# Performance work log

Hardware: AMD Instinct MI355X
Metric: run time of the kernel (lower is better)

## Reference

```python
import jax, jax.numpy as jnp
import numpy as np

KH, KW = 3, 3
STRIDE, PAD, DIL = 1, 1, 1
HEADS, GROUPS, CLIP = 12, 12, 2
C, H, W = 288, 64, 64
B = 2


def _bilinear(img, ys, xs):
    # img: (c, H, W); ys, xs: (K, H, W) fractional sample coords -> (c, K, H, W)
    # DCN-style bilinear with zero outside the image (per-corner validity).
    Hh, Ww = img.shape[1], img.shape[2]
    y0 = jnp.floor(ys)
    x0 = jnp.floor(xs)
    dy = ys - y0
    dx = xs - x0
    out = jnp.zeros((img.shape[0],) + ys.shape, dtype=img.dtype)
    for oy, wy in ((y0, 1.0 - dy), (y0 + 1.0, dy)):
        for ox, wx in ((x0, 1.0 - dx), (x0 + 1.0, dx)):
            valid = (oy >= 0) & (oy <= Hh - 1) & (ox >= 0) & (ox <= Ww - 1)
            yi = jnp.clip(oy, 0, Hh - 1).astype(jnp.int32)
            xi = jnp.clip(ox, 0, Ww - 1).astype(jnp.int32)
            out = out + img[:, yi, xi] * (wy * wx * valid.astype(img.dtype))[None]
    return out


_sample = jax.vmap(jax.vmap(jax.vmap(_bilinear)))  # over (B, T, G)


def _linear5d(x, Wm, b):
    # x: (n, d, c, h, w); Wm: (out, in); torch nn.Linear applied channel-last
    return jnp.einsum('ndchw,oc->ndohw', x, Wm) + b[None, None, :, None, None]


def _deform_attn(q, kv, offset):
    # q: (B,1,C,H,W); kv: (B,T,2C,H,W); offset: (B, T*G*K*2, H, W)
    K = KH * KW
    hd = C // HEADS
    cpg = C // GROUPS
    scale = hd ** -0.5
    A = H * W
    off = offset.reshape(B, CLIP, GROUPS, K, 2, H, W)
    ky = jnp.repeat(jnp.arange(KH), KW).astype(q.dtype)   # (K,)
    kx = jnp.tile(jnp.arange(KW), KH).astype(q.dtype)
    py = jnp.arange(H, dtype=q.dtype)
    px = jnp.arange(W, dtype=q.dtype)
    base_y = ky[:, None, None] * DIL - PAD + py[None, :, None] * STRIDE  # (K,H,1)
    base_x = kx[:, None, None] * DIL - PAD + px[None, None, :] * STRIDE  # (K,1,W)
    ys = base_y + off[..., 0, :, :]  # (B,T,G,K,H,W)
    xs = base_x + off[..., 1, :, :]
    # split kv into k/v, group channels so k and v share per-group offsets
    k_in = kv[:, :, :C].reshape(B, CLIP, GROUPS, cpg, H, W)
    v_in = kv[:, :, C:].reshape(B, CLIP, GROUPS, cpg, H, W)
    kv_g = jnp.concatenate([k_in, v_in], axis=3)          # (B,T,G,2*cpg,H,W)
    samp = _sample(kv_g, ys, xs)                          # (B,T,G,2*cpg,K,H,W)
    k_s = samp[:, :, :, :cpg]
    v_s = samp[:, :, :, cpg:]
    # (B,T,G,cpg,K,H,W) -> (B,HEADS,hd,T*K,A)
    def to_heads(t):
        t = t.reshape(B, CLIP, C, K, A).transpose(0, 2, 1, 3, 4)
        return t.reshape(B, HEADS, hd, CLIP * K, A)
    k_s = to_heads(k_s)
    v_s = to_heads(v_s)
    q_r = q.reshape(B, HEADS, hd, A) * jnp.asarray(scale, q.dtype)
    attn = jnp.einsum('bhda,bhdka->bhka', q_r, k_s)       # (B,HEADS,T*K,A)
    attn = jax.nn.softmax(attn, axis=2)
    out = jnp.einsum('bhka,bhdka->bhda', attn, v_s)
    return out.reshape(B, 1, C, H, W)


def setup_inputs() -> dict:
    key = jax.random.key(0)
    ks = jax.random.split(key, 16)
    s = 0.02
    inp = {
        'q': jax.random.normal(ks[0], (B, 1, C, H, W), jnp.float32),
        'k': jax.random.normal(ks[1], (B, CLIP, C, H, W), jnp.float32),
        'v': jax.random.normal(ks[2], (B, CLIP, C, H, W), jnp.float32),
        'offset': jax.random.normal(ks[3], (B, CLIP * GROUPS * KH * KW * 2, H, W), jnp.float32),
        'Wq': jax.random.normal(ks[4], (C, C), jnp.float32) * s,
        'bq': jnp.zeros((C,), jnp.float32),
        'Wk': jax.random.normal(ks[5], (C, C), jnp.float32) * s,
        'bk': jnp.zeros((C,), jnp.float32),
        'Wv': jax.random.normal(ks[6], (C, C), jnp.float32) * s,
        'bv': jnp.zeros((C,), jnp.float32),
        'W1': jax.random.normal(ks[7], (2 * C, C), jnp.float32) * s,
        'b1': jnp.zeros((2 * C,), jnp.float32),
        'W2': jax.random.normal(ks[8], (C, 2 * C), jnp.float32) * s,
        'b2': jnp.zeros((C,), jnp.float32),
    }
    return inp


def reference(q, k, v, offset, Wq, bq, Wk, bk, Wv, bv, W1, b1, W2, b2):
    qp = _linear5d(q, Wq, bq)
    kv = jnp.concatenate([_linear5d(k, Wk, bk), _linear5d(v, Wv, bv)], axis=2)
    o = _deform_attn(qp, kv, offset)
    # MLP (channel-last), residual: v = v + mlp(v)
    x = jnp.moveaxis(o, 2, -1)
    x = jnp.einsum('ndhwc,oc->ndhwo', x, W1) + b1
    x = jax.nn.gelu(x, approximate=False)
    x = jnp.einsum('ndhwc,oc->ndhwo', x, W2) + b2
    return o + jnp.moveaxis(x, -1, 2)
```

## Files before the change

kernel.cpp:

```cpp
#include <hip/hip_runtime.h>

#define AREA 4096

typedef short short8 __attribute__((ext_vector_type(8)));
typedef float f32x4 __attribute__((ext_vector_type(4)));

__device__ __forceinline__ unsigned bf16_rn(float x) {
    unsigned u = __builtin_bit_cast(unsigned, x);
    u += 0x7fffu + ((u >> 16) & 1u);
    return u >> 16;
}
__device__ __forceinline__ float bflo(unsigned u) { return __builtin_bit_cast(float, u << 16); }
__device__ __forceinline__ float bfhi(unsigned u) { return __builtin_bit_cast(float, u & 0xffff0000u); }
__device__ __forceinline__ float gelu_f(float x) {
    return 0.5f * x * (1.f + erff(x * 0.70710678118654752f));
}

#define OFF_Q 0
#define OFF_K (162 * 64)
#define OFF_V (324 * 64)
#define OFF_1 (486 * 64)
#define OFF_2 (810 * 64)

__global__ __launch_bounds__(256) void prep_kernel(
    const float* __restrict__ q, const float* __restrict__ k,
    const float* __restrict__ v,
    const float* __restrict__ Wq, const float* __restrict__ Wk,
    const float* __restrict__ Wv, const float* __restrict__ W1,
    const float* __restrict__ W2,
    unsigned* __restrict__ xq, unsigned* __restrict__ xk,
    unsigned* __restrict__ xv, uint4* __restrict__ wp)
{
    if (blockIdx.y < 3) {
        const float* src; unsigned* dst; int nimg;
        switch (blockIdx.y) {
            case 0: src = q; dst = xq; nimg = 2; break;
            case 1: src = k; dst = xk; nimg = 4; break;
            default:src = v; dst = xv; nimg = 4; break;
        }
        int idx = blockIdx.x * 256 + threadIdx.x;
        if (idx >= nimg * AREA * 36) return;
        int a = idx & (AREA - 1);
        int rest = idx >> 12;
        int oct = rest % 36;
        int n = rest / 36;
        const float* s = src + ((long)n * 288 + oct * 8) * AREA + a;
        uint4 u;
        u.x = bf16_rn(s[0])        | (bf16_rn(s[AREA])     << 16);
        u.y = bf16_rn(s[2 * AREA]) | (bf16_rn(s[3 * AREA]) << 16);
        u.z = bf16_rn(s[4 * AREA]) | (bf16_rn(s[5 * AREA]) << 16);
        u.w = bf16_rn(s[6 * AREA]) | (bf16_rn(s[7 * AREA]) << 16);
        *(uint4*)(dst + ((long)n * AREA + a) * 144 + oct * 4) = u;
    } else {
        int gw = blockIdx.x * 4 + (threadIdx.x >> 6);
        if (gw >= 1134) return;
        int lane = threadIdx.x & 63;
        const float* W; int Cin, KS, local, off;
        if      (gw < 162) { W = Wq; Cin = 288; KS = 9;  local = gw;       off = OFF_Q; }
        else if (gw < 324) { W = Wk; Cin = 288; KS = 9;  local = gw - 162; off = OFF_K; }
        else if (gw < 486) { W = Wv; Cin = 288; KS = 9;  local = gw - 324; off = OFF_V; }
        else if (gw < 810) { W = W1; Cin = 288; KS = 9;  local = gw - 486; off = OFF_1; }
        else               { W = W2; Cin = 576; KS = 18; local = gw - 810; off = OFF_2; }
        int ot = local / KS, ks = local - ot * KS;
        int o = ot * 16 + (lane & 15);
        int c0 = ks * 32 + ((lane >> 4) << 3);
        const float4* wr = (const float4*)(W + (long)o * Cin + c0);
        float4 f0 = wr[0], f1 = wr[1];
        uint4 u;
        u.x = bf16_rn(f0.x) | (bf16_rn(f0.y) << 16);
        u.y = bf16_rn(f0.z) | (bf16_rn(f0.w) << 16);
        u.z = bf16_rn(f1.x) | (bf16_rn(f1.y) << 16);
        u.w = bf16_rn(f1.z) | (bf16_rn(f1.w) << 16);
        wp[(long)off + (long)local * 64 + lane] = u;
    }
}

__global__ __launch_bounds__(256) void proj_qkv(
    const unsigned* __restrict__ xq, const unsigned* __restrict__ xk,
    const unsigned* __restrict__ xv, const uint4* __restrict__ wp,
    const float* __restrict__ bq, const float* __restrict__ bk,
    const float* __restrict__ bv, unsigned* __restrict__ qp_u,
    unsigned* __restrict__ kv_u)
{
    const int z = blockIdx.z;
    const unsigned* Xt; const uint4* Wp; const float* bias;
    int outmode, voff, n;
    if (z < 2)      { Xt = xq; Wp = wp + OFF_Q; bias = bq; outmode = 1; voff = 0;  n = z; }
    else if (z < 6) { Xt = xk; Wp = wp + OFF_K; bias = bk; outmode = 2; voff = 0;  n = z - 2; }
    else            { Xt = xv; Wp = wp + OFF_V; bias = bv; outmode = 2; voff = 12; n = z - 6; }

    const int tid = threadIdx.x;
    const int lane = tid & 63;
    const int w = tid >> 6;
    const int ot0 = blockIdx.y * 2;
    const int pw = blockIdx.x * 256 + w * 64;
    const int lcol = lane & 15;
    const int lrow = lane >> 4;

    const uint4* xrow[4];
#pragma unroll
    for (int s = 0; s < 4; ++s)
        xrow[s] = (const uint4*)(Xt + ((long)n * AREA + pw + s * 16 + lcol) * 144);
    const uint4* wa0 = Wp + (long)ot0 * 9 * 64 + lane;
    const uint4* wa1 = Wp + (long)(ot0 + 1) * 9 * 64 + lane;

    f32x4 acc[2][4];
#pragma unroll
    for (int m = 0; m < 2; ++m)
#pragma unroll
        for (int s = 0; s < 4; ++s) acc[m][s] = (f32x4){0.f, 0.f, 0.f, 0.f};

    for (int ks = 0; ks < 9; ++ks) {
        uint4 a0 = wa0[(long)ks * 64];
        uint4 a1 = wa1[(long)ks * 64];
        uint4 b[4];
#pragma unroll
        for (int s = 0; s < 4; ++s) b[s] = xrow[s][ks * 4 + lrow];
        short8 A0 = __builtin_bit_cast(short8, a0);
        short8 A1 = __builtin_bit_cast(short8, a1);
#pragma unroll
        for (int s = 0; s < 4; ++s) {
            short8 B = __builtin_bit_cast(short8, b[s]);
            acc[0][s] = __builtin_amdgcn_mfma_f32_16x16x32_bf16(A0, B, acc[0][s], 0, 0, 0);
            acc[1][s] = __builtin_amdgcn_mfma_f32_16x16x32_bf16(A1, B, acc[1][s], 0, 0, 0);
        }
    }

#pragma unroll
    for (int m = 0; m < 2; ++m) {
        const int obase = (ot0 + m) * 16 + lrow * 4;
        const float b0 = bias[obase], b1 = bias[obase + 1];
        const float b2 = bias[obase + 2], b3 = bias[obase + 3];
#pragma unroll
        for (int s = 0; s < 4; ++s) {
            const int pcol = pw + s * 16 + lcol;
            f32x4 a = acc[m][s];
            float v0 = a[0] + b0, v1 = a[1] + b1, v2 = a[2] + b2, v3 = a[3] + b3;
            uint2 st;
            st.x = bf16_rn(v0) | (bf16_rn(v1) << 16);
            st.y = bf16_rn(v2) | (bf16_rn(v3) << 16);
            if (outmode == 1) {
                *(uint2*)(qp_u + ((long)n * AREA + pcol) * 144 + (obase >> 1)) = st;
            } else {
                int g = obase / 24, d0 = obase % 24;
                unsigned* ub = kv_u +
                    ((long)(n * 12 + g) * AREA + pcol) * 24 + voff + (d0 >> 1);
                *(uint2*)ub = st;
            }
        }
    }
}

template<int OUT>
__global__ __launch_bounds__(256) void proj_mfma(
    const unsigned* __restrict__ Xt, const uint4* __restrict__ Wp,
    const float* __restrict__ bias, void* __restrict__ outp,
    const float* __restrict__ res, int KS, int RSu)
{
    const int tid = threadIdx.x;
    const int lane = tid & 63;
    const int w = tid >> 6;
    const int n = blockIdx.z;
    const int ot0 = blockIdx.y * 2;
    const int pw = blockIdx.x * 256 + w * 64;
    const int lcol = lane & 15;
    const int lrow = lane >> 4;

    const uint4* xrow[4];
#pragma unroll
    for (int s = 0; s < 4; ++s)
        xrow[s] = (const uint4*)(Xt + ((long)n * AREA + pw + s * 16 + lcol) * RSu);
    const uint4* wa0 = Wp + (long)ot0 * KS * 64 + lane;
    const uint4* wa1 = Wp + (long)(ot0 + 1) * KS * 64 + lane;

    f32x4 acc[2][4];
#pragma unroll
    for (int m = 0; m < 2; ++m)
#pragma unroll
        for (int s = 0; s < 4; ++s) acc[m][s] = (f32x4){0.f, 0.f, 0.f, 0.f};

    for (int ks = 0; ks < KS; ++ks) {
        uint4 a0 = wa0[(long)ks * 64];
        uint4 a1 = wa1[(long)ks * 64];
        uint4 b[4];
#pragma unroll
        for (int s = 0; s < 4; ++s) b[s] = xrow[s][ks * 4 + lrow];
        short8 A0 = __builtin_bit_cast(short8, a0);
        short8 A1 = __builtin_bit_cast(short8, a1);
#pragma unroll
        for (int s = 0; s < 4; ++s) {
            short8 B = __builtin_bit_cast(short8, b[s]);
            acc[0][s] = __builtin_amdgcn_mfma_f32_16x16x32_bf16(A0, B, acc[0][s], 0, 0, 0);
            acc[1][s] = __builtin_amdgcn_mfma_f32_16x16x32_bf16(A1, B, acc[1][s], 0, 0, 0);
        }
    }

#pragma unroll
    for (int m = 0; m < 2; ++m) {
        const int obase = (ot0 + m) * 16 + lrow * 4;
        const float b0 = bias[obase], b1 = bias[obase + 1];
        const float b2 = bias[obase + 2], b3 = bias[obase + 3];
#pragma unroll
        for (int s = 0; s < 4; ++s) {
            const int pcol = pw + s * 16 + lcol;
            f32x4 a = acc[m][s];
            float v0 = a[0] + b0, v1 = a[1] + b1, v2 = a[2] + b2, v3 = a[3] + b3;
            if (OUT == 3) {
                v0 = gelu_f(v0); v1 = gelu_f(v1); v2 = gelu_f(v2); v3 = gelu_f(v3);
                uint2 st;
                st.x = bf16_rn(v0) | (bf16_rn(v1) << 16);
                st.y = bf16_rn(v2) | (bf16_rn(v3) << 16);
                *(uint2*)((unsigned*)outp + ((long)n * AREA + pcol) * 288 + (obase >> 1)) = st;
            } else {
                float* fb = (float*)outp;
                float vals[4] = {v0, v1, v2, v3};
#pragma unroll
                for (int r = 0; r < 4; ++r) {
                    long addr = ((long)n * 288 + obase + r) * AREA + pcol;
                    fb[addr] = vals[r] + res[addr];
                }
            }
        }
    }
}

__global__ __launch_bounds__(256) void deform_attn_kernel(
    const unsigned* __restrict__ qp, const unsigned* __restrict__ kv,
    const float* __restrict__ offs, float* __restrict__ o,
    unsigned* __restrict__ ot)
{
    const int bid = blockIdx.x;
    const int swz = (bid & 7) * 192 + (bid >> 3);
    const int t = swz * 256 + threadIdx.x;
    const int role = t & 1;
    const int clip = (t >> 1) & 1;
    const int site = t >> 2;
    const int a = site & (AREA - 1);
    const int g = (site >> 12) % 12;
    const int b = site / (12 * AREA);
    const int py = a >> 6, px = a & 63;
    const float scale = 0.20412414523193150818f;

    float qv[24];
    {
        const uint4* qb = (const uint4*)(qp + ((long)b * AREA + a) * 144 + g * 12);
        uint4 q0 = qb[0], q1 = qb[1], q2 = qb[2];
        unsigned uq[12] = {q0.x, q0.y, q0.z, q0.w, q1.x, q1.y, q1.z, q1.w,
                           q2.x, q2.y, q2.z, q2.w};
#pragma unroll
        for (int j = 0; j < 12; ++j) {
            qv[2 * j]     = bflo(uq[j]) * scale;
            qv[2 * j + 1] = bfhi(uq[j]) * scale;
        }
    }

    float m = -1e30f, l = 0.f;
    float outv[24];
#pragma unroll
    for (int d = 0; d < 24; ++d) outv[d] = 0.f;

    const unsigned* __restrict__ cb =
        kv + (long)((b * 2 + clip) * 12 + g) * AREA * 24 + role * 12;
    const float* __restrict__ obase =
        offs + ((long)b * 432 + (clip * 12 + g) * 18) * AREA;
#pragma unroll 1
    for (int k = 0; k < 9; ++k) {
        float oy = obase[(long)(2 * k) * AREA + a];
        float ox = obase[(long)(2 * k + 1) * AREA + a];
        int ky = k / 3, kx = k - ky * 3;
        float ys = (float)(py + ky - 1) + oy;
        float xs_ = (float)(px + kx - 1) + ox;
        float y0f = floorf(ys), x0f = floorf(xs_);
        float dy = ys - y0f, dx = xs_ - x0f;
        float wy[2] = {1.f - dy, dy};
        float wx[2] = {1.f - dx, dx};
        long  idx4[4];
        float w4[4];
#pragma unroll
        for (int cy = 0; cy < 2; ++cy) {
            float yc = y0f + (float)cy;
            bool vy = (yc >= 0.f) && (yc <= 63.f);
            int yi = (int)fminf(fmaxf(yc, 0.f), 63.f);
#pragma unroll
            for (int cx = 0; cx < 2; ++cx) {
                float xc = x0f + (float)cx;
                bool vx = (xc >= 0.f) && (xc <= 63.f);
                int xi = (int)fminf(fmaxf(xc, 0.f), 63.f);
                w4[cy * 2 + cx] = wy[cy] * wx[cx] * ((vy && vx) ? 1.f : 0.f);
                idx4[cy * 2 + cx] = (long)(yi * 64 + xi) * 24;
            }
        }
        float xs[24];
#pragma unroll
        for (int j = 0; j < 24; ++j) xs[j] = 0.f;
        float sh = 0.f;
#pragma unroll
        for (int c = 0; c < 4; ++c) {
            const uint4* pc = (const uint4*)(cb + idx4[c]);
            uint4 u0 = pc[0], u1 = pc[1], u2 = pc[2];
            unsigned uu[12] = {u0.x, u0.y, u0.z, u0.w,
                               u1.x, u1.y, u1.z, u1.w,
                               u2.x, u2.y, u2.z, u2.w};
            float w = w4[c];
            float d = 0.f;
#pragma unroll
            for (int j = 0; j < 12; ++j) {
                float lo = bflo(uu[j]), hi = bfhi(uu[j]);
                d = fmaf(qv[2 * j], lo, d);
                d = fmaf(qv[2 * j + 1], hi, d);
                xs[2 * j]     = fmaf(w, lo, xs[2 * j]);
                xs[2 * j + 1] = fmaf(w, hi, xs[2 * j + 1]);
            }
            sh = fmaf(w, d, sh);
        }
        float sx = __shfl_xor(sh, 1);
        float s = role ? sx : sh;
        float mn = fmaxf(m, s);
        float corr = __expf(m - mn);
        float p = __expf(s - mn);
        l = l * corr + p;
        m = mn;
#pragma unroll
        for (int j = 0; j < 24; ++j)
            outv[j] = fmaf(outv[j], corr, p * xs[j]);
    }

    float mo  = __shfl_xor(m, 2);
    float lo2 = __shfl_xor(l, 2);
    float mn = fmaxf(m, mo);
    float fs = __expf(m - mn), fo = __expf(mo - mn);
    float lm = l * fs + lo2 * fo;
    float inv = 1.f / lm;
#pragma unroll
    for (int d = 0; d < 24; ++d) {
        float ovo = __shfl_xor(outv[d], 2);
        outv[d] = (outv[d] * fs + ovo * fo) * inv;
    }

    if (role == 1 && clip == 0) {
        float ov[24];
#pragma unroll
        for (int d = 0; d < 24; ++d) {
            ov[d] = outv[d];
            o[((long)b * 288 + g * 24 + d) * AREA + a] = ov[d];
        }
        unsigned* tb = ot + ((long)b * AREA + a) * 144 + g * 12;
        uint4 s0, s1, s2;
        s0.x = bf16_rn(ov[0])  | (bf16_rn(ov[1])  << 16);
        s0.y = bf16_rn(ov[2])  | (bf16_rn(ov[3])  << 16);
        s0.z = bf16_rn(ov[4])  | (bf16_rn(ov[5])  << 16);
        s0.w = bf16_rn(ov[6])  | (bf16_rn(ov[7])  << 16);
        s1.x = bf16_rn(ov[8])  | (bf16_rn(ov[9])  << 16);
        s1.y = bf16_rn(ov[10]) | (bf16_rn(ov[11]) << 16);
        s1.z = bf16_rn(ov[12]) | (bf16_rn(ov[13]) << 16);
        s1.w = bf16_rn(ov[14]) | (bf16_rn(ov[15]) << 16);
        s2.x = bf16_rn(ov[16]) | (bf16_rn(ov[17]) << 16);
        s2.y = bf16_rn(ov[18]) | (bf16_rn(ov[19]) << 16);
        s2.z = bf16_rn(ov[20]) | (bf16_rn(ov[21]) << 16);
        s2.w = bf16_rn(ov[22]) | (bf16_rn(ov[23]) << 16);
        ((uint4*)tb)[0] = s0; ((uint4*)tb)[1] = s1; ((uint4*)tb)[2] = s2;
    }
}

extern "C" void kernel_launch(void* const* d_in, const int* in_sizes, int n_in,
                              void* d_out, int out_size, void* d_ws, size_t ws_size,
                              hipStream_t stream) {
    const float* q      = (const float*)d_in[0];
    const float* k      = (const float*)d_in[1];
    const float* v      = (const float*)d_in[2];
    const float* offset = (const float*)d_in[3];
    const float* Wq     = (const float*)d_in[4];
    const float* bq     = (const float*)d_in[5];
    const float* Wk     = (const float*)d_in[6];
    const float* bk     = (const float*)d_in[7];
    const float* Wv     = (const float*)d_in[8];
    const float* bv     = (const float*)d_in[9];
    const float* W1     = (const float*)d_in[10];
    const float* b1     = (const float*)d_in[11];
    const float* W2     = (const float*)d_in[12];
    const float* b2     = (const float*)d_in[13];
    float* out = (float*)d_out;
    float* ws  = (float*)d_ws;

    unsigned* qp_u = (unsigned*)ws;
    unsigned* kv_u = (unsigned*)(ws + 2359296);
    unsigned* xq   = (unsigned*)(ws + 7077888);
    unsigned* xk   = (unsigned*)(ws + 8257536);
    unsigned* xv   = (unsigned*)(ws + 10616832);
    uint4*    wp   = (uint4*)(ws + 12976128);
    unsigned* x1   = xk;
    unsigned* o_t  = xv;

    prep_kernel<<<dim3(2304, 4), dim3(256), 0, stream>>>(
        q, k, v, Wq, Wk, Wv, W1, W2, xq, xk, xv, wp);
    proj_qkv<<<dim3(16, 9, 10), dim3(256), 0, stream>>>(
        xq, xk, xv, wp, bq, bk, bv, qp_u, kv_u);
    deform_attn_kernel<<<dim3(1536), dim3(256), 0, stream>>>(
        qp_u, kv_u, offset, out, o_t);
    proj_mfma<3><<<dim3(16, 18, 2), dim3(256), 0, stream>>>(
        o_t, wp + OFF_1, b1, x1, nullptr, 9, 144);
    proj_mfma<0><<<dim3(16, 9, 2), dim3(256), 0, stream>>>(
        x1, wp + OFF_2, b2, out, out, 18, 288);
}
```

Baseline: 134.0 us.

## Fuse bf16 conversion of inputs and weights into projection GEMMs via LDS staging

Removes the separate prep kernel. The projection kernels now read the fp32 weights and the fp32 q/k/v activations directly, convert them to bf16 and stage them in LDS, transposing activations on the fly. This drops one launch and the write and re-read of the intermediate bf16 buffers, at the cost of redundant weight conversion in every block and extra syncs per k-step in the QKV GEMM. The deform-attention sampling loop is also partially unrolled.

```diff
diff --git a/kernel.cpp b/kernel.cpp
--- a/kernel.cpp
+++ b/kernel.cpp
@@ -16,93 +16,63 @@
     return 0.5f * x * (1.f + erff(x * 0.70710678118654752f));
 }
 
-#define OFF_Q 0
-#define OFF_K (162 * 64)
-#define OFF_V (324 * 64)
-#define OFF_1 (486 * 64)
-#define OFF_2 (810 * 64)
-
-__global__ __launch_bounds__(256) void prep_kernel(
+template<int CIN>
+__device__ __forceinline__ void stage_A(const float* __restrict__ Wrow0,
+                                        unsigned* lds_a, int tid) {
+    const int AW = CIN / 2 + 4;
+    for (int i = tid; i < 32 * CIN / 4; i += 256) {
+        int o = i / (CIN / 4);
+        int c4 = i - o * (CIN / 4);
+        float4 f = *(const float4*)(Wrow0 + (long)o * CIN + c4 * 4);
+        lds_a[o * AW + c4 * 2]     = bf16_rn(f.x) | (bf16_rn(f.y) << 16);
+        lds_a[o * AW + c4 * 2 + 1] = bf16_rn(f.z) | (bf16_rn(f.w) << 16);
+    }
+}
+
+__device__ __forceinline__ void stage_B(const float* __restrict__ Xbase,
+                                        unsigned* lds_b, int tid) {
+#pragma unroll
+    for (int j = 0; j < 4; ++j) {
+        int cpair = j * 4 + (tid >> 6);
+        int px0 = (tid & 63) * 4;
+        const float* r0 = Xbase + (long)(2 * cpair) * AREA + px0;
+        float4 a = *(const float4*)r0;
+        float4 b = *(const float4*)(r0 + AREA);
+        lds_b[(px0 + 0) * 20 + cpair] = bf16_rn(a.x) | (bf16_rn(b.x) << 16);
+        lds_b[(px0 + 1) * 20 + cpair] = bf16_rn(a.y) | (bf16_rn(b.y) << 16);
+        lds_b[(px0 + 2) * 20 + cpair] = bf16_rn(a.z) | (bf16_rn(b.z) << 16);
+        lds_b[(px0 + 3) * 20 + cpair] = bf16_rn(a.w) | (bf16_rn(b.w) << 16);
+    }
+}
+
+__global__ __launch_bounds__(256) void proj_qkv2(
     const float* __restrict__ q, const float* __restrict__ k,
     const float* __restrict__ v,
     const float* __restrict__ Wq, const float* __restrict__ Wk,
-    const float* __restrict__ Wv, const float* __restrict__ W1,
-    const float* __restrict__ W2,
-    unsigned* __restrict__ xq, unsigned* __restrict__ xk,
-    unsigned* __restrict__ xv, uint4* __restrict__ wp)
+    const float* __restrict__ Wv,
+    const float* __restrict__ bq, const float* __restrict__ bk,
+    const float* __restrict__ bv,
+    unsigned* __restrict__ qp_u, unsigned* __restrict__ kv_u)
 {
-    if (blockIdx.y < 3) {
-        const float* src; unsigned* dst; int nimg;
-        switch (blockIdx.y) {
-            case 0: src = q; dst = xq; nimg = 2; break;
-            case 1: src = k; dst = xk; nimg = 4; break;
-            default:src = v; dst = xv; nimg = 4; break;
-        }
-        int idx = blockIdx.x * 256 + threadIdx.x;
-        if (idx >= nimg * AREA * 36) return;
-        int a = idx & (AREA - 1);
-        int rest = idx >> 12;
-        int oct = rest % 36;
-        int n = rest / 36;
-        const float* s = src + ((long)n * 288 + oct * 8) * AREA + a;
-        uint4 u;
-        u.x = bf16_rn(s[0])        | (bf16_rn(s[AREA])     << 16);
-        u.y = bf16_rn(s[2 * AREA]) | (bf16_rn(s[3 * AREA]) << 16);
-        u.z = bf16_rn(s[4 * AREA]) | (bf16_rn(s[5 * AREA]) << 16);
-        u.w = bf16_rn(s[6 * AREA]) | (bf16_rn(s[7 * AREA]) << 16);
-        *(uint4*)(dst + ((long)n * AREA + a) * 144 + oct * 4) = u;
-    } else {
-        int gw = blockIdx.x * 4 + (threadIdx.x >> 6);
-        if (gw >= 1134) return;
-        int lane = threadIdx.x & 63;
-        const float* W; int Cin, KS, local, off;
-        if      (gw < 162) { W = Wq; Cin = 288; KS = 9;  local = gw;       off = OFF_Q; }
-        else if (gw < 324) { W = Wk; Cin = 288; KS = 9;  local = gw - 162; off = OFF_K; }
-        else if (gw < 486) { W = Wv; Cin = 288; KS = 9;  local = gw - 324; off = OFF_V; }
-        else if (gw < 810) { W = W1; Cin = 288; KS = 9;  local = gw - 486; off = OFF_1; }
-        else               { W = W2; Cin = 576; KS = 18; local = gw - 810; off = OFF_2; }
-        int ot = local / KS, ks = local - ot * KS;
-        int o = ot * 16 + (lane & 15);
-        int c0 = ks * 32 + ((lane >> 4) << 3);
-        const float4* wr = (const float4*)(W + (long)o * Cin + c0);
-        float4 f0 = wr[0], f1 = wr[1];
-        uint4 u;
-        u.x = bf16_rn(f0.x) | (bf16_rn(f0.y) << 16);
-        u.y = bf16_rn(f0.z) | (bf16_rn(f0.w) << 16);
-        u.z = bf16_rn(f1.x) | (bf16_rn(f1.y) << 16);
-        u.w = bf16_rn(f1.z) | (bf16_rn(f1.w) << 16);
-        wp[(long)off + (long)local * 64 + lane] = u;
-    }
-}
-
-__global__ __launch_bounds__(256) void proj_qkv(
-    const unsigned* __restrict__ xq, const unsigned* __restrict__ xk,
-    const unsigned* __restrict__ xv, const uint4* __restrict__ wp,
-    const float* __restrict__ bq, const float* __restrict__ bk,
-    const float* __restrict__ bv, unsigned* __restrict__ qp_u,
-    unsigned* __restrict__ kv_u)
-{
+    __shared__ unsigned lds_a[32 * 148];
+    __shared__ unsigned lds_b[256 * 20];
     const int z = blockIdx.z;
-    const unsigned* Xt; const uint4* Wp; const float* bias;
+    const float* Xf; const float* W; const float* bias;
     int outmode, voff, n;
-    if (z < 2)      { Xt = xq; Wp = wp + OFF_Q; bias = bq; outmode = 1; voff = 0;  n = z; }
-    else if (z < 6) { Xt = xk; Wp = wp + OFF_K; bias = bk; outmode = 2; voff = 0;  n = z - 2; }
-    else            { Xt = xv; Wp = wp + OFF_V; bias = bv; outmode = 2; voff = 12; n = z - 6; }
+    if (z < 2)      { Xf = q; W = Wq; bias = bq; outmode = 1; voff = 0;  n = z; }
+    else if (z < 6) { Xf = k; W = Wk; bias = bk; outmode = 2; voff = 0;  n = z - 2; }
+    else            { Xf = v; W = Wv; bias = bv; outmode = 2; voff = 12; n = z - 6; }
 
     const int tid = threadIdx.x;
     const int lane = tid & 63;
     const int w = tid >> 6;
     const int ot0 = blockIdx.y * 2;
-    const int pw = blockIdx.x * 256 + w * 64;
+    const int pwb = blockIdx.x * 256;
     const int lcol = lane & 15;
     const int lrow = lane >> 4;
-
-    const uint4* xrow[4];
-#pragma unroll
-    for (int s = 0; s < 4; ++s)
-        xrow[s] = (const uint4*)(Xt + ((long)n * AREA + pw + s * 16 + lcol) * 144);
-    const uint4* wa0 = Wp + (long)ot0 * 9 * 64 + lane;
-    const uint4* wa1 = Wp + (long)(ot0 + 1) * 9 * 64 + lane;
+    const int AW = 148;
+
+    stage_A<288>(W + (long)blockIdx.y * 32 * 288, lds_a, tid);
 
     f32x4 acc[2][4];
 #pragma unroll
@@ -110,17 +80,19 @@
 #pragma unroll
         for (int s = 0; s < 4; ++s) acc[m][s] = (f32x4){0.f, 0.f, 0.f, 0.f};
 
+    const float* Xn = Xf + (long)n * 288 * AREA + pwb;
     for (int ks = 0; ks < 9; ++ks) {
-        uint4 a0 = wa0[(long)ks * 64];
-        uint4 a1 = wa1[(long)ks * 64];
-        uint4 b[4];
-#pragma unroll
-        for (int s = 0; s < 4; ++s) b[s] = xrow[s][ks * 4 + lrow];
+        __syncthreads();
+        stage_B(Xn + (long)(ks * 32) * AREA, lds_b, tid);
+        __syncthreads();
+        uint4 a0 = *(const uint4*)&lds_a[(0 * 16 + lcol) * AW + ks * 16 + lrow * 4];
+        uint4 a1 = *(const uint4*)&lds_a[(1 * 16 + lcol) * AW + ks * 16 + lrow * 4];
         short8 A0 = __builtin_bit_cast(short8, a0);
         short8 A1 = __builtin_bit_cast(short8, a1);
 #pragma unroll
         for (int s = 0; s < 4; ++s) {
-            short8 B = __builtin_bit_cast(short8, b[s]);
+            uint4 bb = *(const uint4*)&lds_b[(w * 64 + s * 16 + lcol) * 20 + lrow * 4];
+            short8 B = __builtin_bit_cast(short8, bb);
             acc[0][s] = __builtin_amdgcn_mfma_f32_16x16x32_bf16(A0, B, acc[0][s], 0, 0, 0);
             acc[1][s] = __builtin_amdgcn_mfma_f32_16x16x32_bf16(A1, B, acc[1][s], 0, 0, 0);
         }
@@ -133,7 +105,7 @@
         const float b2 = bias[obase + 2], b3 = bias[obase + 3];
 #pragma unroll
         for (int s = 0; s < 4; ++s) {
-            const int pcol = pw + s * 16 + lcol;
+            const int pcol = pwb + w * 64 + s * 16 + lcol;
             f32x4 a = acc[m][s];
             float v0 = a[0] + b0, v1 = a[1] + b1, v2 = a[2] + b2, v3 = a[3] + b3;
             uint2 st;
@@ -143,20 +115,20 @@
                 *(uint2*)(qp_u + ((long)n * AREA + pcol) * 144 + (obase >> 1)) = st;
             } else {
                 int g = obase / 24, d0 = obase % 24;
-                unsigned* ub = kv_u +
-                    ((long)(n * 12 + g) * AREA + pcol) * 24 + voff + (d0 >> 1);
-                *(uint2*)ub = st;
+                *(uint2*)(kv_u + ((long)(n * 12 + g) * AREA + pcol) * 24 + voff + (d0 >> 1)) = st;
             }
         }
     }
 }
 
-template<int OUT>
-__global__ __launch_bounds__(256) void proj_mfma(
-    const unsigned* __restrict__ Xt, const uint4* __restrict__ Wp,
+template<int OUT, int CIN>
+__global__ __launch_bounds__(256) void proj_ffn(
+    const unsigned* __restrict__ Xu, const float* __restrict__ W,
     const float* __restrict__ bias, void* __restrict__ outp,
-    const float* __restrict__ res, int KS, int RSu)
+    const float* __restrict__ res, int RSu)
 {
+    const int AW = CIN / 2 + 4;
+    __shared__ unsigned lds_a[32 * (CIN / 2 + 4)];
     const int tid = threadIdx.x;
     const int lane = tid & 63;
     const int w = tid >> 6;
@@ -166,12 +138,13 @@
     const int lcol = lane & 15;
     const int lrow = lane >> 4;
 
+    stage_A<CIN>(W + (long)blockIdx.y * 32 * CIN, lds_a, tid);
+    __syncthreads();
+
     const uint4* xrow[4];
 #pragma unroll
     for (int s = 0; s < 4; ++s)
-        xrow[s] = (const uint4*)(Xt + ((long)n * AREA + pw + s * 16 + lcol) * RSu);
-    const uint4* wa0 = Wp + (long)ot0 * KS * 64 + lane;
-    const uint4* wa1 = Wp + (long)(ot0 + 1) * KS * 64 + lane;
+        xrow[s] = (const uint4*)(Xu + ((long)n * AREA + pw + s * 16 + lcol) * RSu);
 
     f32x4 acc[2][4];
 #pragma unroll
@@ -179,17 +152,14 @@
 #pragma unroll
         for (int s = 0; s < 4; ++s) acc[m][s] = (f32x4){0.f, 0.f, 0.f, 0.f};
 
-    for (int ks = 0; ks < KS; ++ks) {
-        uint4 a0 = wa0[(long)ks * 64];
-        uint4 a1 = wa1[(long)ks * 64];
-        uint4 b[4];
-#pragma unroll
-        for (int s = 0; s < 4; ++s) b[s] = xrow[s][ks * 4 + lrow];
+    for (int ks = 0; ks < CIN / 32; ++ks) {
+        uint4 a0 = *(const uint4*)&lds_a[(0 * 16 + lcol) * AW + ks * 16 + lrow * 4];
+        uint4 a1 = *(const uint4*)&lds_a[(1 * 16 + lcol) * AW + ks * 16 + lrow * 4];
         short8 A0 = __builtin_bit_cast(short8, a0);
         short8 A1 = __builtin_bit_cast(short8, a1);
 #pragma unroll
         for (int s = 0; s < 4; ++s) {
-            short8 B = __builtin_bit_cast(short8, b[s]);
+            short8 B = __builtin_bit_cast(short8, xrow[s][ks * 4 + lrow]);
             acc[0][s] = __builtin_amdgcn_mfma_f32_16x16x32_bf16(A0, B, acc[0][s], 0, 0, 0);
             acc[1][s] = __builtin_amdgcn_mfma_f32_16x16x32_bf16(A1, B, acc[1][s], 0, 0, 0);
         }
@@ -263,7 +233,7 @@
         kv + (long)((b * 2 + clip) * 12 + g) * AREA * 24 + role * 12;
     const float* __restrict__ obase =
         offs + ((long)b * 432 + (clip * 12 + g) * 18) * AREA;
-#pragma unroll 1
+#pragma unroll 3
     for (int k = 0; k < 9; ++k) {
         float oy = obase[(long)(2 * k) * AREA + a];
         float ox = obase[(long)(2 * k + 1) * AREA + a];
@@ -384,21 +354,15 @@
 
     unsigned* qp_u = (unsigned*)ws;
     unsigned* kv_u = (unsigned*)(ws + 2359296);
-    unsigned* xq   = (unsigned*)(ws + 7077888);
-    unsigned* xk   = (unsigned*)(ws + 8257536);
-    unsigned* xv   = (unsigned*)(ws + 10616832);
-    uint4*    wp   = (uint4*)(ws + 12976128);
-    unsigned* x1   = xk;
-    unsigned* o_t  = xv;
-
-    prep_kernel<<<dim3(2304, 4), dim3(256), 0, stream>>>(
-        q, k, v, Wq, Wk, Wv, W1, W2, xq, xk, xv, wp);
-    proj_qkv<<<dim3(16, 9, 10), dim3(256), 0, stream>>>(
-        xq, xk, xv, wp, bq, bk, bv, qp_u, kv_u);
+    unsigned* o_t  = (unsigned*)(ws + 8257536);
+    unsigned* x1   = (unsigned*)(ws + 10616832);
+
+    proj_qkv2<<<dim3(16, 9, 10), dim3(256), 0, stream>>>(
+        q, k, v, Wq, Wk, Wv, bq, bk, bv, qp_u, kv_u);
     deform_attn_kernel<<<dim3(1536), dim3(256), 0, stream>>>(
         qp_u, kv_u, offset, out, o_t);
-    proj_mfma<3><<<dim3(16, 18, 2), dim3(256), 0, stream>>>(
-        o_t, wp + OFF_1, b1, x1, nullptr, 9, 144);
-    proj_mfma<0><<<dim3(16, 9, 2), dim3(256), 0, stream>>>(
-        x1, wp + OFF_2, b2, out, out, 18, 288);
-}
+    proj_ffn<3, 288><<<dim3(16, 18, 2), dim3(256), 0, stream>>>(
+        o_t, W1, b1, x1, nullptr, 144);
+    proj_ffn<0, 576><<<dim3(16, 9, 2), dim3(256), 0, stream>>>(
+        x1, W2, b2, out, out, 288);
+}
```

Result: slower. 165.4 us (+23.4%).

## Split deformable attention into LDS-staged logits pass and separate value-sum pass

Applied to the files above, without the earlier changes.

The fused deformable-attention kernel is split in two. The first kernel stages one half of a group's key slab (12 channels times 4096 pixels) in shared memory and computes bilinear-sampled partial logits from LDS into a global buffer. The second kernel sums the halves, runs a non-online softmax over the 9 taps per clip, and gathers values from a separate V buffer. K and V are written as separate layouts by the projection kernel. This replaces scattered global gathers for K with LDS gathers and removes the online-softmax rescaling. In exchange it adds a logits round-trip through global memory, repeats the offset and bilinear work in both kernels, adds one more launch, and uses 1024-thread blocks with a large LDS footprint.

```diff
diff --git a/kernel.cpp b/kernel.cpp
--- a/kernel.cpp
+++ b/kernel.cpp
@@ -14,6 +14,30 @@
 __device__ __forceinline__ float bfhi(unsigned u) { return __builtin_bit_cast(float, u & 0xffff0000u); }
 __device__ __forceinline__ float gelu_f(float x) {
     return 0.5f * x * (1.f + erff(x * 0.70710678118654752f));
+}
+
+__device__ __forceinline__ void bilin(int k, int py, int px, float oy, float ox,
+                                      int* idx4, float* w4) {
+    int ky = k / 3, kx = k - ky * 3;
+    float ys = (float)(py + ky - 1) + oy;
+    float xs = (float)(px + kx - 1) + ox;
+    float y0f = floorf(ys), x0f = floorf(xs);
+    float dy = ys - y0f, dx = xs - x0f;
+    float wy[2] = {1.f - dy, dy}, wx[2] = {1.f - dx, dx};
+#pragma unroll
+    for (int cy = 0; cy < 2; ++cy) {
+        float yc = y0f + (float)cy;
+        bool vy = (yc >= 0.f) && (yc <= 63.f);
+        int yi = (int)fminf(fmaxf(yc, 0.f), 63.f);
+#pragma unroll
+        for (int cx = 0; cx < 2; ++cx) {
+            float xc = x0f + (float)cx;
+            bool vx = (xc >= 0.f) && (xc <= 63.f);
+            int xi = (int)fminf(fmaxf(xc, 0.f), 63.f);
+            w4[cy * 2 + cx] = wy[cy] * wx[cx] * ((vy && vx) ? 1.f : 0.f);
+            idx4[cy * 2 + cx] = yi * 64 + xi;
+        }
+    }
 }
 
 #define OFF_Q 0
@@ -80,14 +104,14 @@
     const unsigned* __restrict__ xv, const uint4* __restrict__ wp,
     const float* __restrict__ bq, const float* __restrict__ bk,
     const float* __restrict__ bv, unsigned* __restrict__ qp_u,
-    unsigned* __restrict__ kv_u)
+    unsigned* __restrict__ k_u, unsigned* __restrict__ v_u)
 {
     const int z = blockIdx.z;
     const unsigned* Xt; const uint4* Wp; const float* bias;
-    int outmode, voff, n;
-    if (z < 2)      { Xt = xq; Wp = wp + OFF_Q; bias = bq; outmode = 1; voff = 0;  n = z; }
-    else if (z < 6) { Xt = xk; Wp = wp + OFF_K; bias = bk; outmode = 2; voff = 0;  n = z - 2; }
-    else            { Xt = xv; Wp = wp + OFF_V; bias = bv; outmode = 2; voff = 12; n = z - 6; }
+    int outmode, n;
+    if (z < 2)      { Xt = xq; Wp = wp + OFF_Q; bias = bq; outmode = 0; n = z; }
+    else if (z < 6) { Xt = xk; Wp = wp + OFF_K; bias = bk; outmode = 1; n = z - 2; }
+    else            { Xt = xv; Wp = wp + OFF_V; bias = bv; outmode = 2; n = z - 6; }
 
     const int tid = threadIdx.x;
     const int lane = tid & 63;
@@ -139,13 +163,17 @@
             uint2 st;
             st.x = bf16_rn(v0) | (bf16_rn(v1) << 16);
             st.y = bf16_rn(v2) | (bf16_rn(v3) << 16);
-            if (outmode == 1) {
+            if (outmode == 0) {
                 *(uint2*)(qp_u + ((long)n * AREA + pcol) * 144 + (obase >> 1)) = st;
+            } else if (outmode == 1) {
+                int g = obase / 24, d0 = obase % 24;
+                int half = d0 >= 12 ? 1 : 0;
+                int slab = n * 12 + g;
+                *(uint2*)(k_u + ((long)(slab * 2 + half) * AREA + pcol) * 6
+                          + ((d0 % 12) >> 1)) = st;
             } else {
                 int g = obase / 24, d0 = obase % 24;
-                unsigned* ub = kv_u +
-                    ((long)(n * 12 + g) * AREA + pcol) * 24 + voff + (d0 >> 1);
-                *(uint2*)ub = st;
+                *(uint2*)(v_u + ((long)(n * 12 + g) * AREA + pcol) * 12 + (d0 >> 1)) = st;
             }
         }
     }
@@ -224,140 +252,157 @@
     }
 }
 
-__global__ __launch_bounds__(256) void deform_attn_kernel(
-    const unsigned* __restrict__ qp, const unsigned* __restrict__ kv,
+__global__ __launch_bounds__(1024) void attn_logits(
+    const unsigned* __restrict__ qp, const unsigned* __restrict__ k_u,
+    const float* __restrict__ offs, float* __restrict__ lg)
+{
+    __shared__ unsigned kl[AREA * 6];
+    const int bid = blockIdx.x;
+    const int lid = (bid & 7) * 48 + (bid >> 3);
+    const int chunk = lid & 3;
+    const int half = (lid >> 2) & 1;
+    const int slab = lid >> 3;
+    const int g = slab % 12;
+    const int bc = slab / 12;
+    const int b = bc >> 1, clip = bc & 1;
+    const int tid = threadIdx.x;
+
+    const unsigned* ks = k_u + (long)(slab * 2 + half) * AREA * 6;
+#pragma unroll
+    for (int i = 0; i < 4; ++i) {
+        int px = i * 1024 + tid;
+        uint2 a0 = *(const uint2*)(ks + (long)px * 6);
+        uint2 a1 = *(const uint2*)(ks + (long)px * 6 + 2);
+        uint2 a2 = *(const uint2*)(ks + (long)px * 6 + 4);
+        *(uint2*)&kl[px * 6]     = a0;
+        *(uint2*)&kl[px * 6 + 2] = a1;
+        *(uint2*)&kl[px * 6 + 4] = a2;
+    }
+    __syncthreads();
+
+    const int a = chunk * 1024 + tid;
+    const int py = a >> 6, px = a & 63;
+    const float scale = 0.20412414523193150818f;
+    float qv[12];
+    {
+        const unsigned* qb = qp + ((long)b * AREA + a) * 144 + g * 12 + half * 6;
+#pragma unroll
+        for (int j = 0; j < 6; ++j) {
+            unsigned u = qb[j];
+            qv[2 * j]     = bflo(u) * scale;
+            qv[2 * j + 1] = bfhi(u) * scale;
+        }
+    }
+    const float* ob = offs + ((long)b * 432 + (clip * 12 + g) * 18) * AREA + a;
+    float* lout = lg + ((long)(((b * 12 + g) * 2 + clip) * 2 + half) * 9) * AREA + a;
+
+#pragma unroll 3
+    for (int k = 0; k < 9; ++k) {
+        float oy = ob[(long)(2 * k) * AREA];
+        float ox = ob[(long)(2 * k + 1) * AREA];
+        int idx4[4]; float w4[4];
+        bilin(k, py, px, oy, ox, idx4, w4);
+        float s = 0.f;
+#pragma unroll
+        for (int c = 0; c < 4; ++c) {
+            const unsigned* kc = &kl[idx4[c] * 6];
+            uint2 u0 = *(const uint2*)kc;
+            uint2 u1 = *(const uint2*)(kc + 2);
+            uint2 u2 = *(const uint2*)(kc + 4);
+            float d = qv[0] * bflo(u0.x) + qv[1] * bfhi(u0.x)
+                    + qv[2] * bflo(u0.y) + qv[3] * bfhi(u0.y)
+                    + qv[4] * bflo(u1.x) + qv[5] * bfhi(u1.x)
+                    + qv[6] * bflo(u1.y) + qv[7] * bfhi(u1.y)
+                    + qv[8] * bflo(u2.x) + qv[9] * bfhi(u2.x)
+                    + qv[10] * bflo(u2.y) + qv[11] * bfhi(u2.y);
+            s = fmaf(w4[c], d, s);
+        }
+        lout[(long)k * AREA] = s;
+    }
+}
+
+__global__ __launch_bounds__(256) void attn_vsum(
+    const unsigned* __restrict__ v_u, const float* __restrict__ lg,
     const float* __restrict__ offs, float* __restrict__ o,
     unsigned* __restrict__ ot)
 {
     const int bid = blockIdx.x;
-    const int swz = (bid & 7) * 192 + (bid >> 3);
+    const int swz = (bid & 7) * 96 + (bid >> 3);
     const int t = swz * 256 + threadIdx.x;
-    const int role = t & 1;
-    const int clip = (t >> 1) & 1;
-    const int site = t >> 2;
+    const int clip = t & 1;
+    const int site = t >> 1;
     const int a = site & (AREA - 1);
     const int g = (site >> 12) % 12;
     const int b = site / (12 * AREA);
     const int py = a >> 6, px = a & 63;
-    const float scale = 0.20412414523193150818f;
-
-    float qv[24];
-    {
-        const uint4* qb = (const uint4*)(qp + ((long)b * AREA + a) * 144 + g * 12);
-        uint4 q0 = qb[0], q1 = qb[1], q2 = qb[2];
-        unsigned uq[12] = {q0.x, q0.y, q0.z, q0.w, q1.x, q1.y, q1.z, q1.w,
-                           q2.x, q2.y, q2.z, q2.w};
-#pragma unroll
-        for (int j = 0; j < 12; ++j) {
-            qv[2 * j]     = bflo(uq[j]) * scale;
-            qv[2 * j + 1] = bfhi(uq[j]) * scale;
-        }
-    }
-
-    float m = -1e30f, l = 0.f;
+
+    const float* lbase = lg + ((long)(((b * 12 + g) * 2 + clip) * 2) * 9) * AREA + a;
+    float s9[9];
+    float m9 = -1e30f;
+#pragma unroll
+    for (int k = 0; k < 9; ++k) {
+        s9[k] = lbase[(long)k * AREA] + lbase[(long)(9 + k) * AREA];
+        m9 = fmaxf(m9, s9[k]);
+    }
+    float l9 = 0.f;
+#pragma unroll
+    for (int k = 0; k < 9; ++k) { s9[k] = __expf(s9[k] - m9); l9 += s9[k]; }
+    float mo = __shfl_xor(m9, 1);
+    float lo = __shfl_xor(l9, 1);
+    float M = fmaxf(m9, mo);
+    float fs = __expf(m9 - M);
+    float l = l9 * fs + lo * __expf(mo - M);
+    float winv = fs / l;
+
     float outv[24];
 #pragma unroll
     for (int d = 0; d < 24; ++d) outv[d] = 0.f;
 
-    const unsigned* __restrict__ cb =
-        kv + (long)((b * 2 + clip) * 12 + g) * AREA * 24 + role * 12;
-    const float* __restrict__ obase =
-        offs + ((long)b * 432 + (clip * 12 + g) * 18) * AREA;
-#pragma unroll 1
+    const unsigned* vb = v_u + (long)((b * 2 + clip) * 12 + g) * AREA * 12;
+    const float* ob = offs + ((long)b * 432 + (clip * 12 + g) * 18) * AREA + a;
+#pragma unroll 3
     for (int k = 0; k < 9; ++k) {
-        float oy = obase[(long)(2 * k) * AREA + a];
-        float ox = obase[(long)(2 * k + 1) * AREA + a];
-        int ky = k / 3, kx = k - ky * 3;
-        float ys = (float)(py + ky - 1) + oy;
-        float xs_ = (float)(px + kx - 1) + ox;
-        float y0f = floorf(ys), x0f = floorf(xs_);
-        float dy = ys - y0f, dx = xs_ - x0f;
-        float wy[2] = {1.f - dy, dy};
-        float wx[2] = {1.f - dx, dx};
-        long  idx4[4];
-        float w4[4];
-#pragma unroll
-        for (int cy = 0; cy < 2; ++cy) {
-            float yc = y0f + (float)cy;
-            bool vy = (yc >= 0.f) && (yc <= 63.f);
-            int yi = (int)fminf(fmaxf(yc, 0.f), 63.f);
-#pragma unroll
-            for (int cx = 0; cx < 2; ++cx) {
-                float xc = x0f + (float)cx;
-                bool vx = (xc >= 0.f) && (xc <= 63.f);
-                int xi = (int)fminf(fmaxf(xc, 0.f), 63.f);
-                w4[cy * 2 + cx] = wy[cy] * wx[cx] * ((vy && vx) ? 1.f : 0.f);
-                idx4[cy * 2 + cx] = (long)(yi * 64 + xi) * 24;
-            }
-        }
-        float xs[24];
-#pragma unroll
-        for (int j = 0; j < 24; ++j) xs[j] = 0.f;
-        float sh = 0.f;
+        float oy = ob[(long)(2 * k) * AREA];
+        float ox = ob[(long)(2 * k + 1) * AREA];
+        int idx4[4]; float w4[4];
+        bilin(k, py, px, oy, ox, idx4, w4);
+        float wk = s9[k] * winv;
 #pragma unroll
         for (int c = 0; c < 4; ++c) {
-            const uint4* pc = (const uint4*)(cb + idx4[c]);
+            const uint4* pc = (const uint4*)(vb + (long)idx4[c] * 12);
             uint4 u0 = pc[0], u1 = pc[1], u2 = pc[2];
             unsigned uu[12] = {u0.x, u0.y, u0.z, u0.w,
                                u1.x, u1.y, u1.z, u1.w,
                                u2.x, u2.y, u2.z, u2.w};
-            float w = w4[c];
-            float d = 0.f;
+            float wc = wk * w4[c];
 #pragma unroll
             for (int j = 0; j < 12; ++j) {
-                float lo = bflo(uu[j]), hi = bfhi(uu[j]);
-                d = fmaf(qv[2 * j], lo, d);
-                d = fmaf(qv[2 * j + 1], hi, d);
-                xs[2 * j]     = fmaf(w, lo, xs[2 * j]);
-                xs[2 * j + 1] = fmaf(w, hi, xs[2 * j + 1]);
+                outv[2 * j]     = fmaf(wc, bflo(uu[j]), outv[2 * j]);
+                outv[2 * j + 1] = fmaf(wc, bfhi(uu[j]), outv[2 * j + 1]);
             }
-            sh = fmaf(w, d, sh);
-        }
-        float sx = __shfl_xor(sh, 1);
-        float s = role ? sx : sh;
-        float mn = fmaxf(m, s);
-        float corr = __expf(m - mn);
-        float p = __expf(s - mn);
-        l = l * corr + p;
-        m = mn;
-#pragma unroll
-        for (int j = 0; j < 24; ++j)
-            outv[j] = fmaf(outv[j], corr, p * xs[j]);
-    }
-
-    float mo  = __shfl_xor(m, 2);
-    float lo2 = __shfl_xor(l, 2);
-    float mn = fmaxf(m, mo);
-    float fs = __expf(m - mn), fo = __expf(mo - mn);
-    float lm = l * fs + lo2 * fo;
-    float inv = 1.f / lm;
-#pragma unroll
-    for (int d = 0; d < 24; ++d) {
-        float ovo = __shfl_xor(outv[d], 2);
-        outv[d] = (outv[d] * fs + ovo * fo) * inv;
-    }
-
-    if (role == 1 && clip == 0) {
-        float ov[24];
-#pragma unroll
-        for (int d = 0; d < 24; ++d) {
-            ov[d] = outv[d];
-            o[((long)b * 288 + g * 24 + d) * AREA + a] = ov[d];
-        }
+        }
+    }
+#pragma unroll
+    for (int d = 0; d < 24; ++d) outv[d] += __shfl_xor(outv[d], 1);
+
+    if (clip == 0) {
+#pragma unroll
+        for (int d = 0; d < 24; ++d)
+            o[((long)b * 288 + g * 24 + d) * AREA + a] = outv[d];
         unsigned* tb = ot + ((long)b * AREA + a) * 144 + g * 12;
         uint4 s0, s1, s2;
-        s0.x = bf16_rn(ov[0])  | (bf16_rn(ov[1])  << 16);
-        s0.y = bf16_rn(ov[2])  | (bf16_rn(ov[3])  << 16);
-        s0.z = bf16_rn(ov[4])  | (bf16_rn(ov[5])  << 16);
-        s0.w = bf16_rn(ov[6])  | (bf16_rn(ov[7])  << 16);
-        s1.x = bf16_rn(ov[8])  | (bf16_rn(ov[9])  << 16);
-        s1.y = bf16_rn(ov[10]) | (bf16_rn(ov[11]) << 16);
-        s1.z = bf16_rn(ov[12]) | (bf16_rn(ov[13]) << 16);
-        s1.w = bf16_rn(ov[14]) | (bf16_rn(ov[15]) << 16);
-        s2.x = bf16_rn(ov[16]) | (bf16_rn(ov[17]) << 16);
-        s2.y = bf16_rn(ov[18]) | (bf16_rn(ov[19]) << 16);
-        s2.z = bf16_rn(ov[20]) | (bf16_rn(ov[21]) << 16);
-        s2.w = bf16_rn(ov[22]) | (bf16_rn(ov[23]) << 16);
+        s0.x = bf16_rn(outv[0])  | (bf16_rn(outv[1])  << 16);
+        s0.y = bf16_rn(outv[2])  | (bf16_rn(outv[3])  << 16);
+        s0.z = bf16_rn(outv[4])  | (bf16_rn(outv[5])  << 16);
+        s0.w = bf16_rn(outv[6])  | (bf16_rn(outv[7])  << 16);
+        s1.x = bf16_rn(outv[8])  | (bf16_rn(outv[9])  << 16);
+        s1.y = bf16_rn(outv[10]) | (bf16_rn(outv[11]) << 16);
+        s1.z = bf16_rn(outv[12]) | (bf16_rn(outv[13]) << 16);
+        s1.w = bf16_rn(outv[14]) | (bf16_rn(outv[15]) << 16);
+        s2.x = bf16_rn(outv[16]) | (bf16_rn(outv[17]) << 16);
+        s2.y = bf16_rn(outv[18]) | (bf16_rn(outv[19]) << 16);
+        s2.z = bf16_rn(outv[20]) | (bf16_rn(outv[21]) << 16);
+        s2.w = bf16_rn(outv[22]) | (bf16_rn(outv[23]) << 16);
         ((uint4*)tb)[0] = s0; ((uint4*)tb)[1] = s1; ((uint4*)tb)[2] = s2;
     }
 }
@@ -383,20 +428,22 @@
     float* ws  = (float*)d_ws;
 
     unsigned* qp_u = (unsigned*)ws;
-    unsigned* kv_u = (unsigned*)(ws + 2359296);
-    unsigned* xq   = (unsigned*)(ws + 7077888);
-    unsigned* xk   = (unsigned*)(ws + 8257536);
-    unsigned* xv   = (unsigned*)(ws + 10616832);
-    uint4*    wp   = (uint4*)(ws + 12976128);
-    unsigned* x1   = xk;
-    unsigned* o_t  = xv;
+    unsigned* k_u  = (unsigned*)(ws + 1179648);
+    unsigned* v_u  = (unsigned*)(ws + 3538944);
+    unsigned* xq   = (unsigned*)(ws + 5898240);
+    unsigned* xk   = (unsigned*)(ws + 7077888);
+    unsigned* xv   = (unsigned*)(ws + 9437184);
+    uint4*    wp   = (uint4*)(ws + 11796480);
+    unsigned* o_t  = (unsigned*)(ws + 12086784);
+    float*    lg   = (float*)(ws + 5898240);
+    unsigned* x1   = xv;
 
     prep_kernel<<<dim3(2304, 4), dim3(256), 0, stream>>>(
         q, k, v, Wq, Wk, Wv, W1, W2, xq, xk, xv, wp);
     proj_qkv<<<dim3(16, 9, 10), dim3(256), 0, stream>>>(
-        xq, xk, xv, wp, bq, bk, bv, qp_u, kv_u);
-    deform_attn_kernel<<<dim3(1536), dim3(256), 0, stream>>>(
-        qp_u, kv_u, offset, out, o_t);
+        xq, xk, xv, wp, bq, bk, bv, qp_u, k_u, v_u);
+    attn_logits<<<dim3(384), dim3(1024), 0, stream>>>(qp_u, k_u, offset, lg);
+    attn_vsum<<<dim3(768), dim3(256), 0, stream>>>(v_u, lg, offset, out, o_t);
     proj_mfma<3><<<dim3(16, 18, 2), dim3(256), 0, stream>>>(
         o_t, wp + OFF_1, b1, x1, nullptr, 9, 144);
     proj_mfma<0><<<dim3(16, 9, 2), dim3(256), 0, stream>>>(
```

Result: slower. 149.4 us (+11.5%).
